# Kernel optimization log

Measured on AMD Instinct MI355X. Metric: run time of the kernel, lower is better.

Reference implementation:

```python
import math
import jax, jax.numpy as jnp
import numpy as np

N_WIRES = 12
N_LAYERS = 3
BATCH = 2048
DIM = 2 ** N_WIRES


def _apply_1q(psi, U, wire):
    # psi: (B, 2^n) complex; U: (2,2) or (B,2,2)
    B = psi.shape[0]
    left = 2 ** wire
    psi = psi.reshape(B, left, 2, -1)
    if U.ndim == 3:
        psi = jnp.einsum('bij,bajc->baic', U, psi)
    else:
        psi = jnp.einsum('ij,bajc->baic', U, psi)
    return psi.reshape(B, -1)


def _apply_cnot(psi, wire):
    # CNOT on (control=wire, target=wire+1), adjacent wires
    B = psi.shape[0]
    left = 2 ** wire
    psi = psi.reshape(B, left, 2, 2, -1)
    flipped = psi[:, :, 1, ::-1, :][:, :, None]   # control=1 branch, target flipped
    psi = jnp.concatenate([psi[:, :, 0:1], flipped], axis=2)
    return psi.reshape(B, -1)


def _ry(theta):
    # RY(t) = [[cos t/2, -sin t/2],[sin t/2, cos t/2]]; theta: () or (B,)
    c = jnp.cos(theta / 2)
    s = jnp.sin(theta / 2)
    U = jnp.stack([jnp.stack([c, -s], -1), jnp.stack([s, c], -1)], -2)
    return U.astype(jnp.complex64)


def _rz(theta):
    # RZ(t) = diag(e^{-it/2}, e^{it/2}); theta scalar
    em = jnp.exp(-0.5j * theta.astype(jnp.complex64))
    ep = jnp.exp(0.5j * theta.astype(jnp.complex64))
    e00 = jnp.array([[1, 0], [0, 0]], dtype=jnp.complex64)
    e11 = jnp.array([[0, 0], [0, 1]], dtype=jnp.complex64)
    return e00 * em + e11 * ep


def _measure_z(psi):
    # <Z_w> for every wire; psi: (B, 2^n)
    B = psi.shape[0]
    p = jnp.abs(psi) ** 2
    outs = []
    for w in range(N_WIRES):
        pr = p.reshape(B, 2 ** w, 2, -1)
        outs.append(pr[:, :, 0].sum((1, 2)) - pr[:, :, 1].sum((1, 2)))
    return jnp.stack(outs, axis=-1)  # (B, n_wires)


def _forward(x, W1, b1, ry_theta, rz_theta, W2, b2):
    feat = x @ W1.T + b1                      # (B, n_wires)
    angles = jnp.tanh(feat) * math.pi         # encoding angles
    B = x.shape[0]
    psi = jnp.zeros((B, DIM), dtype=jnp.complex64).at[:, 0].set(1.0)
    # data encoding: per-sample RY on each wire
    for w in range(N_WIRES):
        psi = _apply_1q(psi, _ry(angles[:, w]), w)
    # variational layers with SHARED ry/rz params (module reuse in torch code)
    Ury = _ry(ry_theta)
    Urz = _rz(rz_theta)
    for _ in range(N_LAYERS):
        for w in range(N_WIRES):
            psi = _apply_1q(psi, Ury, w)
            psi = _apply_1q(psi, Urz, w)
        for w in range(N_WIRES - 1):
            psi = _apply_cnot(psi, w)
    z = _measure_z(psi)                        # (B, n_wires) real
    return z @ W2.T + b2                       # (B, 10) logits


def setup_inputs() -> dict:
    key = jax.random.key(0)
    ks = jax.random.split(key, 7)
    return {
        'x': jax.random.normal(ks[0], (BATCH, 784), dtype=jnp.float32),
        'W1': jax.random.normal(ks[1], (N_WIRES, 784), dtype=jnp.float32) * 0.03,
        'b1': jnp.zeros((N_WIRES,), dtype=jnp.float32),
        'ry_theta': jax.random.uniform(ks[2], (), dtype=jnp.float32) * 2 * math.pi,
        'rz_theta': jax.random.uniform(ks[3], (), dtype=jnp.float32) * 2 * math.pi,
        'W2': jax.random.normal(ks[4], (10, N_WIRES), dtype=jnp.float32) * 0.2,
        'b2': jnp.zeros((10,), dtype=jnp.float32),
    }


def reference(x, W1, b1, ry_theta, rz_theta, W2, b2):
    return _forward(x, W1, b1, ry_theta, rz_theta, W2, b2)
```

## Files before the change

### kernel.cpp

```cpp
#include <hip/hip_runtime.h>
#include <math.h>

#define NW   12
#define DIM  4096
#define TPB  256

typedef float v2f __attribute__((ext_vector_type(2)));

template<int CTRL>
__device__ __forceinline__ float fdpp(float v) {
    union { float f; int i; } u, w;
    u.f = v;
    w.i = __builtin_amdgcn_update_dpp(0, u.i, CTRL, 0xF, 0xF, false);
    return w.f;
}

template<int CTRL>
__device__ __forceinline__ float fdpp0(float v) {
    union { float f; int i; } u, w;
    u.f = v;
    w.i = __builtin_amdgcn_update_dpp(0, u.i, CTRL, 0xF, 0xF, true);
    return w.f;
}

__device__ __forceinline__ float wave_red(float v) {
    v += fdpp0<0x111>(v);
    v += fdpp0<0x112>(v);
    v += fdpp0<0x114>(v);
    v += fdpp0<0x118>(v);
    v += fdpp0<0x142>(v);
    v += fdpp0<0x143>(v);
    return v;
}

__device__ __forceinline__ v2f cmulq(v2f a, v2f b) {
    return (v2f){ fmaf(a.x, b.x, -a.y * b.y), fmaf(a.x, b.y, a.y * b.x) };
}

template<int B>
__device__ __forceinline__ void ry_reg(v2f* r, float c, v2f vps, v2f vms) {
#pragma unroll
    for (int p = 0; p < 8; ++p) {
        const int i0 = ((p >> B) << (B + 1)) | (p & ((1 << B) - 1));
        const int i1 = i0 | (1 << B);
        const v2f a = r[i0], b = r[i1];
        r[i0] = __builtin_elementwise_fma(vms, b, a * c);
        r[i1] = __builtin_elementwise_fma(vps, a, b * c);
    }
}

template<int CTRL>
__device__ __forceinline__ void ry_dpp(v2f* r, float c, v2f vsp) {
#pragma unroll
    for (int k = 0; k < 16; ++k) {
        const v2f p = { fdpp<CTRL>(r[k].x), fdpp<CTRL>(r[k].y) };
        r[k] = __builtin_elementwise_fma(vsp, p, r[k] * c);
    }
}

__device__ __forceinline__ void ry_xor4(v2f* r, float c, v2f vsp) {
#pragma unroll
    for (int k = 0; k < 16; ++k) {
        const v2f p = { fdpp<0x141>(fdpp<0x1B>(r[k].x)),
                        fdpp<0x141>(fdpp<0x1B>(r[k].y)) };
        r[k] = __builtin_elementwise_fma(vsp, p, r[k] * c);
    }
}

__global__ __launch_bounds__(TPB, 5)
void qmnist_kernel(const float* __restrict__ x,  const float* __restrict__ W1,
                   const float* __restrict__ b1, const float* __restrict__ ryp,
                   const float* __restrict__ rzp, const float* __restrict__ W2,
                   const float* __restrict__ b2, float* __restrict__ out) {
    __shared__ v2f psi[DIM];
    float* smf  = (float*)psi;
    float* wred = smf;
    float* encc = smf + 48;
    float* encs = smf + 60;
    float* zfin = smf + 72;

    const int tid  = threadIdx.x;
    const int blk  = blockIdx.x;
    const int lane = tid & 63;
    const int wave = tid >> 6;

    float acc[NW];
#pragma unroll
    for (int w = 0; w < NW; ++w) acc[w] = 0.f;
    if (tid < 196) {
        const float4 xv = ((const float4*)(x + (size_t)blk * 784))[tid];
#pragma unroll
        for (int w = 0; w < NW; ++w) {
            const float4 wv = ((const float4*)(W1 + w * 784))[tid];
            acc[w] = fmaf(xv.x, wv.x, fmaf(xv.y, wv.y, fmaf(xv.z, wv.z, xv.w * wv.w)));
        }
    }
#pragma unroll
    for (int w = 0; w < NW; ++w) {
        const float v = wave_red(acc[w]);
        if (lane == 63) wred[wave * NW + w] = v;
    }
    __syncthreads();
    if (tid < NW) {
        float feat = wred[tid] + wred[NW + tid] + wred[2 * NW + tid] + wred[3 * NW + tid] + b1[tid];
        float a = tanhf(feat) * 3.14159265358979323846f;
        float h = 0.5f * a;
        encc[tid] = cosf(h);
        encs[tid] = sinf(h);
    }
    __syncthreads();

    float hi = 1.f;
#pragma unroll
    for (int b = 0; b < 8; ++b)
        hi *= ((tid >> b) & 1) ? encs[11 - b] : encc[11 - b];
    v2f r[16];
#pragma unroll
    for (int k = 0; k < 16; ++k) {
        float f = hi;
        f *= (k & 1) ? encs[3] : encc[3];
        f *= (k & 2) ? encs[2] : encc[2];
        f *= (k & 4) ? encs[1] : encc[1];
        f *= (k & 8) ? encs[0] : encc[0];
        r[k] = (v2f){ f, 0.f };
    }

    const float ry = ryp[0], rz = rzp[0];
    const float c = cosf(0.5f * ry), s = sinf(0.5f * ry);
    const v2f vps = {  s,  s };
    const v2f vms = { -s, -s };
    const int pcT = __popc(tid);
    v2f qv[5], qp[5];
    {
        float sb, cb; __sincosf(rz * (float)(pcT - 6), &sb, &cb);
        float sd, cd; __sincosf(rz, &sd, &cd);
        qv[0] = (v2f){ cb, sb };
        const v2f step = (v2f){ cd, sd };
#pragma unroll
        for (int j = 1; j < 5; ++j) qv[j] = cmulq(qv[j - 1], step);
#pragma unroll
        for (int j = 0; j < 5; ++j) qp[j] = (v2f){ -qv[j].y, qv[j].x };
    }

    const v2f vs0 = (lane & 1) ? vps : vms;
    const v2f vs1 = (lane & 2) ? vps : vms;
    const v2f vs2 = (lane & 4) ? vps : vms;
    const v2f vs3 = (lane & 8) ? vps : vms;

    const int A    = (tid & 15) | ((tid & 240) << 4);
    const int gt   = tid ^ (tid >> 1);
    const int GA1  = A ^ (A >> 1);
    const int GA2  = A ^ (A >> 2);
    const int bs2  = tid ^ (tid >> 2);

#define GREG() { ry_reg<0>(r, c, vps, vms); ry_reg<1>(r, c, vps, vms); \
                 ry_reg<2>(r, c, vps, vms); ry_reg<3>(r, c, vps, vms); }
#define GDPP() { ry_dpp<0xB1>(r, c, vs0); ry_dpp<0x4E>(r, c, vs1); \
                 ry_xor4(r, c, vs2);      ry_dpp<0x128>(r, c, vs3); }
#define RZF()  _Pragma("unroll") for (int k = 0; k < 16; ++k) { \
                 const int j = __popc(k); \
                 r[k] = __builtin_elementwise_fma((v2f){ r[k].y, r[k].y }, qp[j], qv[j] * r[k].x); }
#define S0_Y(k)   (((k) << 8) | tid)
#define S0_A(k)   (A | ((k) << 4))
#define S1_Y(k)   ((gt ^ (((k) & 1) << 7)) | ((((k) ^ ((k) >> 1)) & 15) << 8))
#define S1_A(k)   (GA1 ^ (((k) << 4) ^ ((k) << 3)))
#define S2_Y(k)   (bs2 ^ (((k) & 3) << 6) ^ ((((k) ^ ((k) >> 2)) & 15) << 8))
#define S2_A(k)   (GA2 ^ (((k) << 4) ^ ((k) << 2)))

    __syncthreads();
    GREG();
#pragma unroll
    for (int k = 0; k < 16; ++k) psi[S0_Y(k)] = r[k];
    __syncthreads();
#pragma unroll
    for (int k = 0; k < 16; ++k) r[k] = psi[S0_A(k)];
    GDPP();
    GREG();
    RZF();
#pragma unroll
    for (int k = 0; k < 16; ++k) psi[S0_A(k)] = r[k];
    __syncthreads();
#pragma unroll
    for (int k = 0; k < 16; ++k) r[k] = psi[S1_Y(k)];

    GREG();
#pragma unroll
    for (int k = 0; k < 16; ++k) psi[S1_Y(k)] = r[k];
    __syncthreads();
#pragma unroll
    for (int k = 0; k < 16; ++k) r[k] = psi[S1_A(k)];
    GDPP();
    GREG();
    RZF();
#pragma unroll
    for (int k = 0; k < 16; ++k) psi[S1_A(k)] = r[k];
    __syncthreads();
#pragma unroll
    for (int k = 0; k < 16; ++k) r[k] = psi[S2_Y(k)];

    GREG();
#pragma unroll
    for (int k = 0; k < 16; ++k) psi[S2_Y(k)] = r[k];
    __syncthreads();
#pragma unroll
    for (int k = 0; k < 16; ++k) r[k] = psi[S2_A(k)];
    GDPP();
    GREG();
    __syncthreads();

    float T = 0.f, Sp = 0.f, S1 = 0.f, S2 = 0.f, S3 = 0.f;
#pragma unroll
    for (int k = 0; k < 16; ++k) {
        const float pp = fmaf(r[k].x, r[k].x, r[k].y * r[k].y);
        T += pp;
        Sp += (__popc(k) & 1)        ? -pp : pp;
        S1 += (__popc(k >> 1) & 1)   ? -pp : pp;
        S2 += (__popc(k >> 2) & 1)   ? -pp : pp;
        S3 += ((k >> 3) & 1)         ? -pp : pp;
    }
    const int t1 = (tid >> 1) & 1, t2 = (tid >> 2) & 1, t3 = (tid >> 3) & 1;
    const int t4 = (tid >> 4) & 1, t5 = (tid >> 5) & 1, t6 = (tid >> 6) & 1,
              t7 = (tid >> 7) & 1;
    const int p47 = t4 ^ t5 ^ t6 ^ t7;
    float contrib[NW];
    contrib[0]  = t7                   ? -T : T;
    contrib[1]  = (t6 ^ t7)            ? -T : T;
    contrib[2]  = (t5 ^ t6 ^ t7)       ? -T : T;
    contrib[3]  = p47                  ? -T : T;
    contrib[4]  = p47                  ? -S3 : S3;
    contrib[5]  = p47                  ? -S2 : S2;
    contrib[6]  = p47                  ? -S1 : S1;
    contrib[7]  = p47                  ? -Sp : Sp;
    contrib[8]  = (t3 ^ p47)           ? -Sp : Sp;
    contrib[9]  = (t2 ^ t3 ^ p47)      ? -Sp : Sp;
    contrib[10] = (t1 ^ t2 ^ t3 ^ p47) ? -Sp : Sp;
    contrib[11] = (pcT & 1)            ? -Sp : Sp;
#pragma unroll
    for (int w = 0; w < NW; ++w) {
        const float v = wave_red(contrib[w]);
        if (lane == 63) wred[wave * NW + w] = v;
    }
    __syncthreads();
    if (tid < NW)
        zfin[tid] = wred[tid] + wred[NW + tid] + wred[2 * NW + tid] + wred[3 * NW + tid];
    __syncthreads();

    if (tid < 10) {
        float o = b2[tid];
#pragma unroll
        for (int w = 0; w < NW; ++w)
            o = fmaf(zfin[w], W2[tid * NW + w], o);
        out[(size_t)blk * 10 + tid] = o;
    }
}

extern "C" void kernel_launch(void* const* d_in, const int* in_sizes, int n_in,
                              void* d_out, int out_size, void* d_ws, size_t ws_size,
                              hipStream_t stream) {
    const float* x   = (const float*)d_in[0];
    const float* W1  = (const float*)d_in[1];
    const float* b1  = (const float*)d_in[2];
    const float* ry  = (const float*)d_in[3];
    const float* rz  = (const float*)d_in[4];
    const float* W2  = (const float*)d_in[5];
    const float* b2  = (const float*)d_in[6];
    float* out = (float*)d_out;

    const int batch = in_sizes[0] / 784;
    qmnist_kernel<<<batch, TPB, 0, stream>>>(x, W1, b1, ry, rz, W2, b2, out);
}
```

Before: 110.5 us.

## Split feature projection into a separate per-sample-wave prepass kernel

Moves the x@W1 projection, tanh and cos/sin encoding into a separate kernel that handles one sample per wave and writes 24 floats per sample to the workspace. The main simulation kernel then just loads these values, which removes the projection phase and one barrier from each block. A fallback path keeps the fused version when no workspace is available. The cost is an extra kernel launch plus a global round trip, and the main kernel may still be dominated by the state-vector simulation.

```diff
diff --git a/kernel.cpp b/kernel.cpp
--- a/kernel.cpp
+++ b/kernel.cpp
@@ -67,11 +67,53 @@
     }
 }
 
+__global__ __launch_bounds__(256, 2)
+void feat_kernel(const float* __restrict__ x, const float* __restrict__ W1,
+                 const float* __restrict__ b1, float* __restrict__ ws) {
+    const int lane = threadIdx.x & 63;
+    const int s    = blockIdx.x * 4 + (threadIdx.x >> 6);
+    const float4* xr = (const float4*)(x + (size_t)s * 784);
+    float acc[NW];
+#pragma unroll
+    for (int w = 0; w < NW; ++w) acc[w] = 0.f;
+#pragma unroll
+    for (int i = 0; i < 3; ++i) {
+        const int j = lane + 64 * i;
+        const float4 xv = xr[j];
+#pragma unroll
+        for (int w = 0; w < NW; ++w) {
+            const float4 wv = ((const float4*)(W1 + w * 784))[j];
+            acc[w] = fmaf(xv.x, wv.x, fmaf(xv.y, wv.y, fmaf(xv.z, wv.z, fmaf(xv.w, wv.w, acc[w]))));
+        }
+    }
+    if (lane < 4) {
+        const int j = 192 + lane;
+        const float4 xv = xr[j];
+#pragma unroll
+        for (int w = 0; w < NW; ++w) {
+            const float4 wv = ((const float4*)(W1 + w * 784))[j];
+            acc[w] = fmaf(xv.x, wv.x, fmaf(xv.y, wv.y, fmaf(xv.z, wv.z, fmaf(xv.w, wv.w, acc[w]))));
+        }
+    }
+#pragma unroll
+    for (int w = 0; w < NW; ++w) {
+        const float v = wave_red(acc[w]);
+        if (lane == 63) {
+            const float a = tanhf(v + b1[w]) * 3.14159265358979323846f;
+            const float h = 0.5f * a;
+            ws[(size_t)s * 24 + w]      = cosf(h);
+            ws[(size_t)s * 24 + 12 + w] = sinf(h);
+        }
+    }
+}
+
+template<bool PRE>
 __global__ __launch_bounds__(TPB, 5)
 void qmnist_kernel(const float* __restrict__ x,  const float* __restrict__ W1,
                    const float* __restrict__ b1, const float* __restrict__ ryp,
                    const float* __restrict__ rzp, const float* __restrict__ W2,
-                   const float* __restrict__ b2, float* __restrict__ out) {
+                   const float* __restrict__ b2, float* __restrict__ out,
+                   const float* __restrict__ feats) {
     __shared__ v2f psi[DIM];
     float* smf  = (float*)psi;
     float* wred = smf;
@@ -84,31 +126,36 @@
     const int lane = tid & 63;
     const int wave = tid >> 6;
 
-    float acc[NW];
-#pragma unroll
-    for (int w = 0; w < NW; ++w) acc[w] = 0.f;
-    if (tid < 196) {
-        const float4 xv = ((const float4*)(x + (size_t)blk * 784))[tid];
+    if constexpr (PRE) {
+        if (tid < 24) smf[48 + tid] = feats[(size_t)blk * 24 + tid];
+        __syncthreads();
+    } else {
+        float acc[NW];
+#pragma unroll
+        for (int w = 0; w < NW; ++w) acc[w] = 0.f;
+        if (tid < 196) {
+            const float4 xv = ((const float4*)(x + (size_t)blk * 784))[tid];
+#pragma unroll
+            for (int w = 0; w < NW; ++w) {
+                const float4 wv = ((const float4*)(W1 + w * 784))[tid];
+                acc[w] = fmaf(xv.x, wv.x, fmaf(xv.y, wv.y, fmaf(xv.z, wv.z, xv.w * wv.w)));
+            }
+        }
 #pragma unroll
         for (int w = 0; w < NW; ++w) {
-            const float4 wv = ((const float4*)(W1 + w * 784))[tid];
-            acc[w] = fmaf(xv.x, wv.x, fmaf(xv.y, wv.y, fmaf(xv.z, wv.z, xv.w * wv.w)));
-        }
-    }
-#pragma unroll
-    for (int w = 0; w < NW; ++w) {
-        const float v = wave_red(acc[w]);
-        if (lane == 63) wred[wave * NW + w] = v;
-    }
-    __syncthreads();
-    if (tid < NW) {
-        float feat = wred[tid] + wred[NW + tid] + wred[2 * NW + tid] + wred[3 * NW + tid] + b1[tid];
-        float a = tanhf(feat) * 3.14159265358979323846f;
-        float h = 0.5f * a;
-        encc[tid] = cosf(h);
-        encs[tid] = sinf(h);
-    }
-    __syncthreads();
+            const float v = wave_red(acc[w]);
+            if (lane == 63) wred[wave * NW + w] = v;
+        }
+        __syncthreads();
+        if (tid < NW) {
+            float feat = wred[tid] + wred[NW + tid] + wred[2 * NW + tid] + wred[3 * NW + tid] + b1[tid];
+            float a = tanhf(feat) * 3.14159265358979323846f;
+            float h = 0.5f * a;
+            encc[tid] = cosf(h);
+            encs[tid] = sinf(h);
+        }
+        __syncthreads();
+    }
 
     float hi = 1.f;
 #pragma unroll
@@ -267,5 +314,12 @@
     float* out = (float*)d_out;
 
     const int batch = in_sizes[0] / 784;
-    qmnist_kernel<<<batch, TPB, 0, stream>>>(x, W1, b1, ry, rz, W2, b2, out);
-}
+    if (d_ws != nullptr && ws_size >= (size_t)batch * 24 * sizeof(float)) {
+        feat_kernel<<<batch / 4, 256, 0, stream>>>(x, W1, b1, (float*)d_ws);
+        qmnist_kernel<true><<<batch, TPB, 0, stream>>>(x, W1, b1, ry, rz, W2, b2, out,
+                                                       (const float*)d_ws);
+    } else {
+        qmnist_kernel<false><<<batch, TPB, 0, stream>>>(x, W1, b1, ry, rz, W2, b2, out,
+                                                        nullptr);
+    }
+}
```

Measured after the change: 114.3 us. +3.5%, slower.
